# Performance work log

Measured on AMD Instinct MI355X. Metric: run time of the kernel, lower is better.

The kernel has to match this reference:

```python
import jax, jax.numpy as jnp
import numpy as np
from collections import deque

N, IN_DIM, H, B, L = 512, 64, 128, 256, 2
SOURCE = 105
E_UND = 2048


def _build_graph_and_masks():
    rng = np.random.default_rng(0)
    s = rng.integers(0, N, E_UND)
    d = rng.integers(0, N, E_UND)
    edge_index = np.stack([np.concatenate([s, d]), np.concatenate([d, s])]).astype(np.int32)
    # BFS depths from source (undirected)
    adj = [[] for _ in range(N)]
    for a, b in zip(edge_index[0], edge_index[1]):
        adj[int(a)].append(int(b))
    depths = np.full(N, np.inf)
    depths[SOURCE] = 0.0
    q = deque([SOURCE]); seen = {SOURCE}
    while q:
        u = q.popleft()
        for v in adj[u]:
            if v not in seen:
                seen.add(v); depths[v] = depths[u] + 1.0; q.append(v)
    finite = np.isfinite(depths)
    maxd = depths[finite].max() if finite.any() else 0.0
    depths[~finite] = maxd + 1.0
    adj_mask = np.zeros((N, N), np.float32)
    adj_mask[edge_index[0], edge_index[1]] = 1.0
    adj_mask[edge_index[1], edge_index[0]] = 1.0
    np.fill_diagonal(adj_mask, 1.0)
    direction_mask = (depths[None, :] <= depths[:, None]).astype(np.float32)
    # admittance_matrix is None -> uniform init, then masked
    initial_causal = (np.ones((N, N), np.float32) / N) * adj_mask * direction_mask
    return edge_index, adj_mask, direction_mask, initial_causal


def setup_inputs() -> dict:
    key = jax.random.key(0)
    ks = jax.random.split(key, 16)
    edge_index, adj_mask, direction_mask, initial_causal = _build_graph_and_masks()
    w = lambda k, shp: jax.random.normal(k, shp, jnp.float32) * 0.02
    return {
        'x': jax.random.normal(ks[0], (B, N, IN_DIM), jnp.float32),
        'edge_index': jnp.asarray(edge_index),
        'adj_mask': jnp.asarray(adj_mask),
        'direction_mask': jnp.asarray(direction_mask),
        'causal_logits': jnp.asarray(initial_causal),  # nn.Parameter init
        'W_in': w(ks[1], (IN_DIM, H)), 'b_in': jnp.zeros((H,), jnp.float32),
        'Wq': w(ks[2], (H, H)), 'bq': jnp.zeros((H,), jnp.float32),
        'Wk': w(ks[3], (H, H)), 'bk': jnp.zeros((H,), jnp.float32),
        'Wv': w(ks[4], (H, H)), 'bv': jnp.zeros((H,), jnp.float32),
        'gcn_W': w(ks[5], (L, H, H)), 'gcn_b': jnp.zeros((L, H), jnp.float32),
        'W_fuse': w(ks[6], (2 * H, H)), 'b_fuse': jnp.zeros((H,), jnp.float32),
        'ln_g': jnp.ones((H,), jnp.float32), 'ln_b': jnp.zeros((H,), jnp.float32),
    }


def reference(x, edge_index, adj_mask, direction_mask, causal_logits,
              W_in, b_in, Wq, bq, Wk, bk, Wv, bv,
              gcn_W, gcn_b, W_fuse, b_fuse, ln_g, ln_b):
    n = adj_mask.shape[0]
    h = jax.nn.relu(x @ W_in + b_in)                               # (B,N,H)

    # causal matrix: softmax over learned logits, physically masked, renormalized
    C = jax.nn.softmax(causal_logits, axis=-1) * adj_mask * direction_mask
    C = C / jnp.clip(C.sum(-1, keepdims=True), 1e-8)

    # masked causal attention
    Q = h @ Wq + bq; K = h @ Wk + bk; V = h @ Wv + bv
    scale = jnp.asarray(h.shape[-1] ** 0.5, h.dtype)
    attn = jax.nn.softmax(jnp.einsum('bnh,bmh->bnm', Q, K) / scale, axis=-1)
    attn = attn * C[None]
    attn = attn / (attn.sum(-1, keepdims=True) + 1e-8)
    h_causal = jnp.einsum('bnm,bmh->bnh', attn, V)

    # GCNConv stack (self-loops + symmetric norm; dropout is identity in eval)
    src = jnp.concatenate([edge_index[0], jnp.arange(n, dtype=edge_index.dtype)])
    dst = jnp.concatenate([edge_index[1], jnp.arange(n, dtype=edge_index.dtype)])
    deg = jnp.zeros((n,), h.dtype).at[dst].add(1.0)
    dinv = deg ** -0.5                                              # deg>=1 (self loops)
    norm = (dinv[src] * dinv[dst])[None, :, None]                   # (1,E+N,1)
    h_g = h
    for l in range(gcn_W.shape[0]):
        hW = h_g @ gcn_W[l]                                         # (B,N,H)
        msg = hW[:, src, :] * norm                                  # (B,E+N,H)
        h_g = jnp.zeros_like(hW).at[:, dst, :].add(msg) + gcn_b[l]
        h_g = jax.nn.relu(h_g)

    h_comb = jnp.concatenate([h_causal, h_g], axis=-1) @ W_fuse + b_fuse
    mu = h_comb.mean(-1, keepdims=True)
    var = ((h_comb - mu) ** 2).mean(-1, keepdims=True)
    out = (h_comb - mu) / jnp.sqrt(var + 1e-5) * ln_g + ln_b
    return out, C
```

## Files before the change

### kernel.cpp

```cpp
#include <hip/hip_runtime.h>
#include <hip/hip_bf16.h>
#include <math.h>

#define NN 512
#define HH 128
#define INDIM 64
#define BB 256
#define NE 4096
#define MROWS (BB*NN)
#define OUT0 (BB*NN*HH)

typedef __attribute__((ext_vector_type(8))) short short8v;
typedef __attribute__((ext_vector_type(4))) float float4v;

__device__ __forceinline__ unsigned short f2bf(float f) {
  unsigned u = __float_as_uint(f);
  unsigned r = (u + 0x7fffu + ((u >> 16) & 1u)) >> 16;
  return (unsigned short)r;
}
__device__ __forceinline__ float bf2f(unsigned short b) {
  return __uint_as_float(((unsigned)b) << 16);
}

__global__ __launch_bounds__(256) void k_causalC(
    const float* __restrict__ logits, const float* __restrict__ adj,
    const float* __restrict__ dir, float* __restrict__ Cout)
{
  const int row = blockIdx.x;
  const int t = threadIdx.x;
  __shared__ float red[256];
  const float* lrow = logits + (size_t)row * NN;
  float v0 = lrow[t], v1 = lrow[t + 256];
  float mx = fmaxf(v0, v1);
  red[t] = mx; __syncthreads();
  for (int s = 128; s > 0; s >>= 1) { if (t < s) red[t] = fmaxf(red[t], red[t + s]); __syncthreads(); }
  mx = red[0]; __syncthreads();
  float e0 = __expf(v0 - mx), e1 = __expf(v1 - mx);
  red[t] = e0 + e1; __syncthreads();
  for (int s = 128; s > 0; s >>= 1) { if (t < s) red[t] += red[t + s]; __syncthreads(); }
  float sumE = red[0]; __syncthreads();
  float m0 = adj[(size_t)row * NN + t] * dir[(size_t)row * NN + t];
  float m1 = adj[(size_t)row * NN + t + 256] * dir[(size_t)row * NN + t + 256];
  float me0 = e0 * m0, me1 = e1 * m1;
  red[t] = me0 + me1; __syncthreads();
  for (int s = 128; s > 0; s >>= 1) { if (t < s) red[t] += red[t + s]; __syncthreads(); }
  float sumME = red[0];
  float sm = sumME / sumE;
  float denom = fmaxf(sm, 1e-8f) * sumE;
  Cout[(size_t)row * NN + t]       = me0 / denom;
  Cout[(size_t)row * NN + t + 256] = me1 / denom;
}

__global__ __launch_bounds__(512) void k_csr(const int* __restrict__ ei,
                                             int* __restrict__ rp,
                                             int* __restrict__ ci,
                                             float* __restrict__ cw)
{
  __shared__ int scnt[512];
  __shared__ float sdinv[512];
  __shared__ int sval[512];
  __shared__ int scur[512];
  const int t = threadIdx.x;
  const int* src = ei;
  const int* dst = ei + NE;
  scnt[t] = 0;
  __syncthreads();
  for (int e = t; e < NE; e += 512) atomicAdd(&scnt[dst[e]], 1);
  __syncthreads();
  const int deg = scnt[t] + 1;
  sdinv[t] = rsqrtf((float)deg);
  sval[t] = deg;
  __syncthreads();
  for (int off = 1; off < 512; off <<= 1) {
    int add = (t >= off) ? sval[t - off] : 0;
    __syncthreads();
    sval[t] += add;
    __syncthreads();
  }
  const int excl = sval[t] - deg;
  rp[t] = excl;
  if (t == 511) rp[512] = excl + deg;
  ci[excl] = t;
  cw[excl] = sdinv[t] * sdinv[t];
  scur[t] = excl + 1;
  __syncthreads();
  for (int e = t; e < NE; e += 512) {
    int s = src[e], d = dst[e];
    int p = atomicAdd(&scur[d], 1);
    ci[p] = s;
    cw[p] = sdinv[s] * sdinv[d];
  }
}

__global__ __launch_bounds__(512) void k_ccsr(const int* __restrict__ ei,
                                              const float* __restrict__ Cmat,
                                              int* __restrict__ rp,
                                              int* __restrict__ ci,
                                              float* __restrict__ cw)
{
  __shared__ unsigned bm[512 * 16];
  __shared__ int cnt[512];
  __shared__ int sval[512];
  __shared__ int cur[512];
  const int t = threadIdx.x;
  const int* src = ei;
  const int* dst = ei + NE;
  for (int i = t; i < 512 * 16; i += 512) bm[i] = 0u;
  __syncthreads();
  bm[t * 16 + (t >> 5)] |= (1u << (t & 31));
  cnt[t] = 1;
  __syncthreads();
  for (int e = t; e < NE; e += 512) {
    int r = src[e], c = dst[e];
    if (Cmat[(size_t)r * NN + c] > 0.f) {
      unsigned bit = 1u << (c & 31);
      unsigned old = atomicOr(&bm[r * 16 + (c >> 5)], bit);
      if (!(old & bit)) atomicAdd(&cnt[r], 1);
    }
  }
  __syncthreads();
  const int myc = cnt[t];
  sval[t] = myc;
  __syncthreads();
  for (int off = 1; off < 512; off <<= 1) {
    int add = (t >= off) ? sval[t - off] : 0;
    __syncthreads();
    sval[t] += add;
    __syncthreads();
  }
  const int excl = sval[t] - myc;
  rp[t] = excl;
  if (t == 511) rp[512] = excl + myc;
  ci[excl] = t;
  cw[excl] = Cmat[(size_t)t * NN + t];
  cur[t] = excl + 1;
  bm[t * 16 + (t >> 5)] &= ~(1u << (t & 31));
  __syncthreads();
  for (int e = t; e < NE; e += 512) {
    int r = src[e], c = dst[e];
    if (Cmat[(size_t)r * NN + c] > 0.f) {
      unsigned bit = 1u << (c & 31);
      unsigned old = atomicAnd(&bm[r * 16 + (c >> 5)], ~bit);
      if (old & bit) {
        int p = atomicAdd(&cur[r], 1);
        ci[p] = c;
        cw[p] = Cmat[(size_t)r * NN + c];
      }
    }
  }
}

__device__ __forceinline__ void gcn_body(
    int bid, const unsigned short* __restrict__ hW,
    const int* __restrict__ rp, const int* __restrict__ ci,
    const float* __restrict__ cw, const float* __restrict__ bias,
    unsigned short* __restrict__ out, int OS, int OC0)
{
  const int i5 = bid >> 3;
  const int ng = i5 & 31;
  const int b = (bid & 7) * 32 + (i5 >> 5);
  const int t = threadIdx.x;
  const int node = ng * 16 + (t >> 4);
  const int f0 = (t & 15) * 8;

  float bcol[8];
  #pragma unroll
  for (int k = 0; k < 8; k++) bcol[k] = bias[f0 + k];

  const unsigned short* base = hW + (size_t)b * 512 * 128;
  const int beg = rp[node], end = rp[node + 1];
  float acc[8] = {0.f, 0.f, 0.f, 0.f, 0.f, 0.f, 0.f, 0.f};
  for (int j = beg; j < end; j++) {
    int s = ci[j];
    float w = cw[j];
    short8v v = *(const short8v*)&base[(size_t)s * 128 + f0];
    #pragma unroll
    for (int k = 0; k < 8; k++) acc[k] += w * bf2f((unsigned short)v[k]);
  }
  short8v o;
  #pragma unroll
  for (int k = 0; k < 8; k++) {
    float v = fmaxf(acc[k] + bcol[k], 0.f);
    o[k] = (short)f2bf(v);
  }
  *(short8v*)&out[((size_t)(b * 512 + node)) * OS + OC0 + f0] = o;
}

__global__ __launch_bounds__(256) void k_gcn(
    const unsigned short* __restrict__ hW,
    const int* __restrict__ rp, const int* __restrict__ ci,
    const float* __restrict__ cw, const float* __restrict__ bias,
    unsigned short* __restrict__ out, int OS, int OC0)
{
  gcn_body(blockIdx.x, hW, rp, ci, cw, bias, out, OS, OC0);
}

__device__ __forceinline__ void sattn_body(
    int bid, const unsigned short* __restrict__ Qbf,
    const unsigned short* __restrict__ Kbf, const unsigned short* __restrict__ Vbf,
    const int* __restrict__ rp, const int* __restrict__ ci,
    const float* __restrict__ cw, unsigned short* __restrict__ Ocb)
{
  const int i5 = bid >> 3;
  const int ng = i5 & 31;
  const int b = (bid & 7) * 32 + (i5 >> 5);
  const int t = threadIdx.x;
  const int node = ng * 16 + (t >> 4);
  const int f0 = (t & 15) * 8;
  const float scale = 0.088388347648318447f;

  const size_t rowq = ((size_t)(b * 512 + node)) * 128 + f0;
  short8v qv = *(const short8v*)&Qbf[rowq];
  float qf[8];
  #pragma unroll
  for (int k = 0; k < 8; k++) qf[k] = bf2f((unsigned short)qv[k]);

  const unsigned short* Kb = Kbf + (size_t)b * 512 * 128;
  const unsigned short* Vb = Vbf + (size_t)b * 512 * 128;
  const int beg = rp[node], end = rp[node + 1];
  float acc[8] = {0.f, 0.f, 0.f, 0.f, 0.f, 0.f, 0.f, 0.f};
  float sw = 0.f;
  int j = beg;
  float w0 = cw[j];
  int m = ci[j];
  short8v kv = *(const short8v*)&Kb[(size_t)m * 128 + f0];
  short8v vv = *(const short8v*)&Vb[(size_t)m * 128 + f0];
  for (; j < end; ) {
    const int jn = (j + 1 < end) ? j + 1 : j;
    const float w02 = cw[jn];
    const int m2 = ci[jn];
    short8v kv2 = *(const short8v*)&Kb[(size_t)m2 * 128 + f0];
    short8v vv2 = *(const short8v*)&Vb[(size_t)m2 * 128 + f0];
    float part = 0.f;
    #pragma unroll
    for (int k = 0; k < 8; k++) part += qf[k] * bf2f((unsigned short)kv[k]);
    part += __shfl_xor(part, 1);
    part += __shfl_xor(part, 2);
    part += __shfl_xor(part, 4);
    part += __shfl_xor(part, 8);
    float w = __expf(part * scale) * w0;
    sw += w;
    #pragma unroll
    for (int k = 0; k < 8; k++) acc[k] += w * bf2f((unsigned short)vv[k]);
    j++;
    w0 = w02; kv = kv2; vv = vv2;
  }
  float inv = 1.0f / sw;
  short8v o;
  #pragma unroll
  for (int k = 0; k < 8; k++) o[k] = (short)f2bf(acc[k] * inv);
  *(short8v*)&Ocb[((size_t)(b * 512 + node)) * 256 + f0] = o;
}

__global__ __launch_bounds__(256) void k_gs(
    const unsigned short* __restrict__ hW,
    const int* __restrict__ grp, const int* __restrict__ gci,
    const float* __restrict__ gcw, const float* __restrict__ gbias,
    const unsigned short* __restrict__ Qbf, const unsigned short* __restrict__ Kbf,
    const unsigned short* __restrict__ Vbf,
    const int* __restrict__ arp, const int* __restrict__ aci,
    const float* __restrict__ acw,
    unsigned short* __restrict__ Dout)
{
  if (blockIdx.x < 8192)
    gcn_body(blockIdx.x, hW, grp, gci, gcw, gbias, Dout, 256, 128);
  else
    sattn_body(blockIdx.x - 8192, Qbf, Kbf, Vbf, arp, aci, acw, Dout);
}

__global__ __launch_bounds__(256) void k_wt(
    const float* s0, const float* s1, const float* s2, const float* s3,
    const float* s4, const float* s5, const float* s6,
    unsigned short* d0, unsigned short* d1, unsigned short* d2, unsigned short* d3,
    unsigned short* d4, unsigned short* d5, unsigned short* d6)
{
  const float* srcs[7] = {s0, s1, s2, s3, s4, s5, s6};
  unsigned short* dsts[7] = {d0, d1, d2, d3, d4, d5, d6};
  const int Ks[7] = {64, 128, 128, 128, 128, 128, 256};
  const int j = blockIdx.x >> 3;
  const int nc = blockIdx.x & 7;
  const float* s = srcs[j];
  unsigned short* d = dsts[j];
  const int K = Ks[j];
  const int STRW = K + 8;
  const int n0 = nc * 16;
  __shared__ short tile[16 * 264];
  const int t = threadIdx.x;
  for (int i = t; i < K * 16; i += 256) {
    int k = i >> 4, nn = i & 15;
    tile[nn * STRW + k] = (short)f2bf(s[k * 128 + n0 + nn]);
  }
  __syncthreads();
  for (int i = t; i < K * 2; i += 256) {
    int nn = (i * 8) / K;
    int k  = (i * 8) % K;
    *(short8v*)&d[(size_t)(n0 + nn) * K + k] =
        *(const short8v*)&tile[nn * STRW + k];
  }
}

template<bool RELU>
__global__ __launch_bounds__(512) void k_wgemm(
    const unsigned short* __restrict__ Abf,
    const unsigned short* __restrict__ Wt,
    const float* __restrict__ bias,
    unsigned short* __restrict__ Out)
{
  constexpr int STR = 136;
  __shared__ short Ws[128 * STR];
  __shared__ short rep[8 * 2048];
  const int t = threadIdx.x;
  const int wave = t >> 6, lane = t & 63;
  const int l15 = lane & 15, quad = lane >> 4;
  short* rw = rep + wave * 2048;

  for (int i = t; i < 128 * 16; i += 512) {
    int n = i >> 4, seg = i & 15;
    *(short8v*)&Ws[n * STR + seg * 8] =
        *(const short8v*)&Wt[(size_t)n * 128 + seg * 8];
  }
  float bcol[8];
  #pragma unroll
  for (int nt = 0; nt < 8; nt++) bcol[nt] = bias ? bias[nt * 16 + l15] : 0.f;
  __syncthreads();

  const int nwaves = gridDim.x * 8;
  int tile = blockIdx.x * 8 + wave;
  short8v af[4], afn[4];
  if (tile < MROWS / 16) {
    #pragma unroll
    for (int dc = 0; dc < 4; dc++)
      af[dc] = *(const short8v*)&Abf[((size_t)(tile * 16 + l15)) * 128 + dc * 32 + quad * 8];
  }
  while (tile < MROWS / 16) {
    const int ntile = tile + nwaves;
    if (ntile < MROWS / 16) {
      #pragma unroll
      for (int dc = 0; dc < 4; dc++)
        afn[dc] = *(const short8v*)&Abf[((size_t)(ntile * 16 + l15)) * 128 + dc * 32 + quad * 8];
    }
    float4v acc[8];
    #pragma unroll
    for (int nt = 0; nt < 8; nt++) acc[nt] = (float4v){0.f, 0.f, 0.f, 0.f};
    #pragma unroll
    for (int k32 = 0; k32 < 4; k32++) {
      #pragma unroll
      for (int nt = 0; nt < 8; nt++) {
        short8v wf = *(const short8v*)&Ws[(nt * 16 + l15) * STR + k32 * 32 + quad * 8];
        acc[nt] = __builtin_amdgcn_mfma_f32_16x16x32_bf16(af[k32], wf, acc[nt], 0, 0, 0);
      }
    }
    #pragma unroll
    for (int nt = 0; nt < 8; nt++)
      #pragma unroll
      for (int r = 0; r < 4; r++) {
        float v = acc[nt][r] + bcol[nt];
        if (RELU) v = fmaxf(v, 0.f);
        rw[(quad * 4 + r) * 128 + nt * 16 + l15] = (short)f2bf(v);
      }
    asm volatile("s_waitcnt lgkmcnt(0)" ::: "memory");
    __builtin_amdgcn_sched_barrier(0);
    #pragma unroll
    for (int p = 0; p < 4; p++) {
      int row16 = (lane >> 4) + p * 4, seg = lane & 15;
      short8v vv = *(const short8v*)&rw[row16 * 128 + seg * 8];
      *(short8v*)&Out[((size_t)(tile * 16 + row16)) * 128 + seg * 8] = vv;
    }
    tile = ntile;
    #pragma unroll
    for (int dc = 0; dc < 4; dc++) af[dc] = afn[dc];
  }
}

#define GNT 4
template<int KD, bool RELU, bool BATCHW, int OMODE, bool AF32>
__global__ __launch_bounds__(256) void k_bgemm(
    const void* __restrict__ Ap, const unsigned short* __restrict__ Wt,
    const float* __restrict__ bias, void* __restrict__ Out, int OS,
    const float* __restrict__ lng, const float* __restrict__ lnb)
{
  constexpr int KCH = (KD < 128) ? KD : 128;
  constexpr int STR = KCH + 8;
  constexpr bool WONCE = (KD <= 128);
  constexpr int ASH = (64 * STR > 8192) ? 64 * STR : 8192;
  constexpr int TRIPS = KCH / 32;
  __shared__ short lds[ASH + 128 * STR];
  short* As = lds;
  short* Ws = lds + ASH;
  const unsigned short* Abf = (const unsigned short*)Ap;
  const float* Af = (const float*)Ap;
  const int t = threadIdx.x;
  const int wave = t >> 6, lane = t & 63;
  const int l15 = lane & 15, quad = lane >> 4;

  short8v ap[TRIPS];
  float4 fa[TRIPS], fb[TRIPS];

  auto LOADC = [&](int rb, int kc) {
    #pragma unroll
    for (int j = 0; j < TRIPS; j++) {
      int i = t + j * 256;
      int r = i / (KCH / 8), seg = i % (KCH / 8);
      if (AF32) {
        const float* sp = &Af[(size_t)(rb + r) * KD + kc + seg * 8];
        fa[j] = *(const float4*)sp;
        fb[j] = *(const float4*)(sp + 4);
      } else {
        int arow = BATCHW ? ((rb & 511) + r) : (rb + r);
        ap[j] = *(const short8v*)&Abf[(size_t)arow * KD + kc + seg * 8];
      }
    }
  };
  auto STOREC = [&]() {
    #pragma unroll
    for (int j = 0; j < TRIPS; j++) {
      int i = t + j * 256;
      int r = i / (KCH / 8), seg = i % (KCH / 8);
      if (AF32) {
        short8v pk;
        pk[0] = (short)f2bf(fa[j].x); pk[1] = (short)f2bf(fa[j].y);
        pk[2] = (short)f2bf(fa[j].z); pk[3] = (short)f2bf(fa[j].w);
        pk[4] = (short)f2bf(fb[j].x); pk[5] = (short)f2bf(fb[j].y);
        pk[6] = (short)f2bf(fb[j].z); pk[7] = (short)f2bf(fb[j].w);
        *(short8v*)&As[r * STR + seg * 8] = pk;
      } else {
        *(short8v*)&As[r * STR + seg * 8] = ap[j];
      }
    }
  };

  float bcol[8];
  #pragma unroll
  for (int nt = 0; nt < 8; nt++) bcol[nt] = bias ? bias[nt * 16 + l15] : 0.f;
  float gcol[8], bbcol[8];
  if (OMODE == 2) {
    #pragma unroll
    for (int nt = 0; nt < 8; nt++) { gcol[nt] = lng[nt * 16 + l15]; bbcol[nt] = lnb[nt * 16 + l15]; }
  }

  for (int g = blockIdx.x; g < (MROWS / 64) / GNT; g += gridDim.x) {
    if (WONCE) {
      const int b0 = (g * GNT * 64) >> 9;
      const unsigned short* Wb = BATCHW ? (Wt + (size_t)b0 * 128 * KD) : Wt;
      for (int i = t; i < 128 * (KCH / 8); i += 256) {
        int n = i / (KCH / 8), seg = i % (KCH / 8);
        *(short8v*)&Ws[n * STR + seg * 8] =
            *(const short8v*)&Wb[(size_t)n * KD + seg * 8];
      }
    }
    LOADC(g * GNT * 64, 0);
    for (int tt = 0; tt < GNT; tt++) {
      const int tile = g * GNT + tt;
      const int rowbase = tile * 64;
      const int b = rowbase >> 9;
      float4v acc[8];
      #pragma unroll
      for (int nt = 0; nt < 8; nt++) acc[nt] = (float4v){0.f, 0.f, 0.f, 0.f};

      for (int kc = 0; kc < KD; kc += KCH) {
        __syncthreads();
        STOREC();
        if (!WONCE) {
          const unsigned short* Wb = BATCHW ? (Wt + (size_t)b * 128 * KD) : Wt;
          for (int i = t; i < 128 * (KCH / 8); i += 256) {
            int n = i / (KCH / 8), seg = i % (KCH / 8);
            *(short8v*)&Ws[n * STR + seg * 8] =
                *(const short8v*)&Wb[(size_t)n * KD + kc + seg * 8];
          }
        }
        __syncthreads();
        {
          int nkc = kc + KCH, ntt = tt;
          if (nkc >= KD) { nkc = 0; ntt = tt + 1; }
          if (ntt < GNT) LOADC((g * GNT + ntt) * 64, nkc);
        }
        #pragma unroll
        for (int k32 = 0; k32 < KCH / 32; k32++) {
          short8v af = *(const short8v*)&As[(wave * 16 + l15) * STR + k32 * 32 + quad * 8];
          #pragma unroll
          for (int nt = 0; nt < 8; nt++) {
            short8v wf = *(const short8v*)&Ws[(nt * 16 + l15) * STR + k32 * 32 + quad * 8];
            acc[nt] = __builtin_amdgcn_mfma_f32_16x16x32_bf16(af, wf, acc[nt], 0, 0, 0);
          }
        }
      }

      __syncthreads();
      if (OMODE == 0) {
        short* rep = As + wave * 2048;
        #pragma unroll
        for (int nt = 0; nt < 8; nt++)
          #pragma unroll
          for (int r = 0; r < 4; r++) {
            float v = acc[nt][r] + bcol[nt];
            if (RELU) v = fmaxf(v, 0.f);
            rep[(quad * 4 + r) * 128 + nt * 16 + l15] = (short)f2bf(v);
          }
        __syncthreads();
        unsigned short* Ob = (unsigned short*)Out;
        #pragma unroll
        for (int p = 0; p < 4; p++) {
          int row16 = (lane >> 4) + p * 4, seg = lane & 15;
          short8v vv = *(const short8v*)&rep[row16 * 128 + seg * 8];
          *(short8v*)&Ob[(size_t)(rowbase + wave * 16 + row16) * OS + seg * 8] = vv;
        }
      } else if (OMODE == 1) {
        short* rep = As + wave * 2048;
        #pragma unroll
        for (int nt = 0; nt < 8; nt++)
          #pragma unroll
          for (int r = 0; r < 4; r++) {
            float v = acc[nt][r] + bcol[nt];
            if (RELU) v = fmaxf(v, 0.f);
            rep[(nt * 16 + l15) * 16 + quad * 4 + r] = (short)f2bf(v);
          }
        __syncthreads();
        unsigned short* Ob = (unsigned short*)Out;
        int node0 = (rowbase & 511) + wave * 16;
        #pragma unroll
        for (int p = 0; p < 4; p++) {
          int idx = p * 64 + lane, c = idx >> 1, half = idx & 1;
          short8v vv = *(const short8v*)&rep[c * 16 + half * 8];
          *(short8v*)&Ob[((size_t)(b * 128 + c)) * 512 + node0 + half * 8] = vv;
        }
      } else {
        float* repw = (float*)lds + wave * 2048;
        float vv[8][4];
        float s[4] = {0, 0, 0, 0}, ss[4] = {0, 0, 0, 0};
        #pragma unroll
        for (int nt = 0; nt < 8; nt++)
          #pragma unroll
          for (int r = 0; r < 4; r++) {
            float v = acc[nt][r] + bcol[nt];
            vv[nt][r] = v;
            s[r] += v; ss[r] += v * v;
          }
        #pragma unroll
        for (int r = 0; r < 4; r++) {
          s[r] += __shfl_xor(s[r], 1);  s[r] += __shfl_xor(s[r], 2);
          s[r] += __shfl_xor(s[r], 4);  s[r] += __shfl_xor(s[r], 8);
          ss[r] += __shfl_xor(ss[r], 1); ss[r] += __shfl_xor(ss[r], 2);
          ss[r] += __shfl_xor(ss[r], 4); ss[r] += __shfl_xor(ss[r], 8);
        }
        #pragma unroll
        for (int r = 0; r < 4; r++) {
          float mu = s[r] * (1.0f / 128.0f);
          float var = ss[r] * (1.0f / 128.0f) - mu * mu;
          float inv = rsqrtf(var + 1e-5f);
          #pragma unroll
          for (int nt = 0; nt < 8; nt++)
            repw[(quad * 4 + r) * 128 + nt * 16 + l15] =
                (vv[nt][r] - mu) * inv * gcol[nt] + bbcol[nt];
        }
        __syncthreads();
        float* Of = (float*)Out;
        #pragma unroll
        for (int p = 0; p < 8; p++) {
          int row16 = (lane >> 5) + p * 2, seg = lane & 31;
          float4 o = *(const float4*)&repw[row16 * 128 + seg * 4];
          *(float4*)&Of[(size_t)(rowbase + wave * 16 + row16) * 128 + seg * 4] = o;
        }
      }
    }
  }
}

__global__ __launch_bounds__(512) void k_hqkv4(
    const float* __restrict__ x,
    const unsigned short* __restrict__ Wint,
    const float* __restrict__ bin,
    const unsigned short* __restrict__ W0, const unsigned short* __restrict__ W1,
    const unsigned short* __restrict__ W2, const unsigned short* __restrict__ W3,
    const float* __restrict__ b1, const float* __restrict__ b2,
    const float* __restrict__ b3,
    unsigned short* __restrict__ O0, unsigned short* __restrict__ O1,
    unsigned short* __restrict__ O2, unsigned short* __restrict__ O3)
{
  constexpr int STR = 136;
  constexpr int RSTR = 136;
  __shared__ short Ws[128 * STR];
  __shared__ short rep[8 * 2304];
  const int t = threadIdx.x;
  const int wave = t >> 6, lane = t & 63;
  const int l15 = lane & 15, quad = lane >> 4;
  short* rw = rep + wave * 2304;

  const unsigned short* Wsrc[4] = {W0, W1, W2, W3};
  const float* Bsrc[4] = {nullptr, b1, b2, b3};
  unsigned short* Osrc[4] = {O0, O1, O2, O3};

  float bh[8];
  #pragma unroll
  for (int nt = 0; nt < 8; nt++) bh[nt] = bin[nt * 16 + l15];

  for (int g = blockIdx.x; g < MROWS / 256; g += gridDim.x) {
    __syncthreads();
    for (int i = t; i < 128 * 8; i += 512) {
      int n = i >> 3, seg = i & 7;
      *(short8v*)&Ws[n * STR + seg * 8] =
          *(const short8v*)&Wint[(size_t)n * 64 + seg * 8];
    }
    __syncthreads();

    short8v af_all[2][4];
    #pragma unroll
    for (int tt = 0; tt < 2; tt++) {
      const int row0 = (g * 2 + tt) * 128 + wave * 16;
      const float* xp = &x[(size_t)(row0 + l15) * 64 + quad * 16];
      float4 fx0 = *(const float4*)(xp);
      float4 fx1 = *(const float4*)(xp + 4);
      float4 fx2 = *(const float4*)(xp + 8);
      float4 fx3 = *(const float4*)(xp + 12);
      short8v px0, px1;
      px0[0] = (short)f2bf(fx0.x); px0[1] = (short)f2bf(fx0.y);
      px0[2] = (short)f2bf(fx0.z); px0[3] = (short)f2bf(fx0.w);
      px0[4] = (short)f2bf(fx1.x); px0[5] = (short)f2bf(fx1.y);
      px0[6] = (short)f2bf(fx1.z); px0[7] = (short)f2bf(fx1.w);
      px1[0] = (short)f2bf(fx2.x); px1[1] = (short)f2bf(fx2.y);
      px1[2] = (short)f2bf(fx2.z); px1[3] = (short)f2bf(fx2.w);
      px1[4] = (short)f2bf(fx3.x); px1[5] = (short)f2bf(fx3.y);
      px1[6] = (short)f2bf(fx3.z); px1[7] = (short)f2bf(fx3.w);
      *(short8v*)&rw[l15 * 72 + quad * 16]     = px0;
      *(short8v*)&rw[l15 * 72 + quad * 16 + 8] = px1;
      asm volatile("s_waitcnt lgkmcnt(0)" ::: "memory");
      __builtin_amdgcn_sched_barrier(0);

      float4v hacc[8];
      #pragma unroll
      for (int nt = 0; nt < 8; nt++) hacc[nt] = (float4v){0.f, 0.f, 0.f, 0.f};
      #pragma unroll
      for (int k32 = 0; k32 < 2; k32++) {
        short8v ax = *(const short8v*)&rw[l15 * 72 + k32 * 32 + quad * 8];
        #pragma unroll
        for (int nt = 0; nt < 8; nt++) {
          short8v wf = *(const short8v*)&Ws[(nt * 16 + l15) * STR + k32 * 32 + quad * 8];
          hacc[nt] = __builtin_amdgcn_mfma_f32_16x16x32_bf16(ax, wf, hacc[nt], 0, 0, 0);
        }
      }
      #pragma unroll
      for (int nt = 0; nt < 8; nt++)
        #pragma unroll
        for (int r = 0; r < 4; r++) {
          float v = fmaxf(hacc[nt][r] + bh[nt], 0.f);
          rw[(quad * 4 + r) * RSTR + nt * 16 + l15] = (short)f2bf(v);
        }
      asm volatile("s_waitcnt lgkmcnt(0)" ::: "memory");
      __builtin_amdgcn_sched_barrier(0);
      #pragma unroll
      for (int dc = 0; dc < 4; dc++)
        af_all[tt][dc] = *(const short8v*)&rw[l15 * RSTR + dc * 32 + quad * 8];
    }

    #pragma unroll
    for (int s = 0; s < 4; s++) {
      __syncthreads();
      for (int i = t; i < 128 * 16; i += 512) {
        int n = i >> 4, seg = i & 15;
        *(short8v*)&Ws[n * STR + seg * 8] =
            *(const short8v*)&Wsrc[s][(size_t)n * 128 + seg * 8];
      }
      float bcol[8];
      #pragma unroll
      for (int nt = 0; nt < 8; nt++) bcol[nt] = Bsrc[s] ? Bsrc[s][nt * 16 + l15] : 0.f;
      __syncthreads();

      #pragma unroll
      for (int tt = 0; tt < 2; tt++) {
        const int rowbase = (g * 2 + tt) * 128;
        float4v acc[8];
        #pragma unroll
        for (int nt = 0; nt < 8; nt++) acc[nt] = (float4v){0.f, 0.f, 0.f, 0.f};
        #pragma unroll
        for (int k32 = 0; k32 < 4; k32++) {
          #pragma unroll
          for (int nt = 0; nt < 8; nt++) {
            short8v wf = *(const short8v*)&Ws[(nt * 16 + l15) * STR + k32 * 32 + quad * 8];
            acc[nt] = __builtin_amdgcn_mfma_f32_16x16x32_bf16(af_all[tt][k32], wf, acc[nt], 0, 0, 0);
          }
        }
        #pragma unroll
        for (int nt = 0; nt < 8; nt++)
          #pragma unroll
          for (int r = 0; r < 4; r++) {
            float v = acc[nt][r] + bcol[nt];
            rw[(quad * 4 + r) * RSTR + nt * 16 + l15] = (short)f2bf(v);
          }
        asm volatile("s_waitcnt lgkmcnt(0)" ::: "memory");
        __builtin_amdgcn_sched_barrier(0);
        unsigned short* Ob = Osrc[s];
        #pragma unroll
        for (int p = 0; p < 4; p++) {
          int row16 = (lane >> 4) + p * 4, seg = lane & 15;
          short8v vv = *(const short8v*)&rw[row16 * RSTR + seg * 8];
          *(short8v*)&Ob[(size_t)(rowbase + wave * 16 + row16) * 128 + seg * 8] = vv;
        }
      }
    }
  }
}

extern "C" void kernel_launch(void* const* d_in, const int* in_sizes, int n_in,
                              void* d_out, int out_size, void* d_ws, size_t ws_size,
                              hipStream_t stream)
{
  const float* x     = (const float*)d_in[0];
  const int*   ei    = (const int*)d_in[1];
  const float* adj   = (const float*)d_in[2];
  const float* dmask = (const float*)d_in[3];
  const float* clog  = (const float*)d_in[4];
  const float* W_in  = (const float*)d_in[5];
  const float* b_in  = (const float*)d_in[6];
  const float* Wq    = (const float*)d_in[7];
  const float* bq    = (const float*)d_in[8];
  const float* Wk    = (const float*)d_in[9];
  const float* bk    = (const float*)d_in[10];
  const float* Wv    = (const float*)d_in[11];
  const float* bv    = (const float*)d_in[12];
  const float* gcnW  = (const float*)d_in[13];
  const float* gcnB  = (const float*)d_in[14];
  const float* Wf    = (const float*)d_in[15];
  const float* bf    = (const float*)d_in[16];
  const float* lng   = (const float*)d_in[17];
  const float* lnb   = (const float*)d_in[18];

  float* outp = (float*)d_out;
  float* Cmat = outp + OUT0;

  char* W = (char*)d_ws;
  const size_t SLOT = (size_t)MROWS * 128 * 2;
  unsigned short* A0 = (unsigned short*)(W);
  unsigned short* B0 = (unsigned short*)(W + SLOT);
  unsigned short* C0 = (unsigned short*)(W + 2 * SLOT);
  unsigned short* D0 = (unsigned short*)(W + 3 * SLOT);
  char* AUX = W + 5 * SLOT;
  int*   csr_rp = (int*)AUX;
  int*   csr_ci = csr_rp + 640;
  float* csr_cw = (float*)(csr_ci + 4608);
  int*   crp    = (int*)(AUX + 131072);
  int*   cci    = crp + 640;
  float* ccw    = (float*)(cci + 8192);
  unsigned short* WB    = (unsigned short*)(AUX + 512 * 512 * 4) + 512 * 512 * 2;
  unsigned short* W_int = WB;
  unsigned short* Wqt   = WB + 8192;
  unsigned short* Wkt   = Wqt + 16384;
  unsigned short* Wvt   = Wkt + 16384;
  unsigned short* G0t   = Wvt + 16384;
  unsigned short* G1t   = G0t + 16384;
  unsigned short* Wft   = G1t + 16384;

  unsigned short* Vbf = (unsigned short*)outp;
  unsigned short* E0  = Vbf + (size_t)MROWS * 128;

  k_causalC<<<512, 256, 0, stream>>>(clog, adj, dmask, Cmat);
  k_csr<<<1, 512, 0, stream>>>(ei, csr_rp, csr_ci, csr_cw);
  k_ccsr<<<1, 512, 0, stream>>>(ei, Cmat, crp, cci, ccw);
  k_wt<<<56, 256, 0, stream>>>(W_in, Wq, Wk, Wv, gcnW, gcnW + HH * HH, Wf,
                               W_int, Wqt, Wkt, Wvt, G0t, G1t, Wft);

  k_hqkv4<<<512, 512, 0, stream>>>(
      x, W_int, b_in, G0t, Wqt, Wkt, Wvt, bq, bk, bv, A0, C0, E0, Vbf);
  k_gcn<<<8192, 256, 0, stream>>>(A0, csr_rp, csr_ci, csr_cw, gcnB, B0, 128, 0);
  k_wgemm<false><<<512, 512, 0, stream>>>(B0, G1t, nullptr, A0);
  k_gs<<<16384, 256, 0, stream>>>(
      A0, csr_rp, csr_ci, csr_cw, gcnB + HH,
      C0, E0, Vbf, crp, cci, ccw, D0);
  k_bgemm<256, false, false, 2, false><<<512, 256, 0, stream>>>(
      D0, Wft, bf, outp, 128, lng, lnb);
}
```

Baseline: 364.5 us.

## Replace fusion GEMM+LayerNorm with wave-tiled kernel holding full weight in LDS

Replaces the templated block GEMM used for the fuse projection plus LayerNorm with a dedicated kernel. It loads the whole 128x256 weight into LDS once per block and has each wave own 16-row tiles, reading A fragments straight from global into registers. This removes per-tile syncthreads, A staging through LDS and the LDS repack before stores, at the cost of uncoalesced scalar fp32 output writes. The GCN gather loop is also software-pipelined to prefetch the next neighbor row.

Result: slower. 406.5 us (+11.5%).

```diff
diff --git a/kernel.cpp b/kernel.cpp
--- a/kernel.cpp
+++ b/kernel.cpp
@@ -170,18 +170,25 @@
   const unsigned short* base = hW + (size_t)b * 512 * 128;
   const int beg = rp[node], end = rp[node + 1];
   float acc[8] = {0.f, 0.f, 0.f, 0.f, 0.f, 0.f, 0.f, 0.f};
-  for (int j = beg; j < end; j++) {
-    int s = ci[j];
-    float w = cw[j];
-    short8v v = *(const short8v*)&base[(size_t)s * 128 + f0];
+  int j = beg;
+  float w = cw[j];
+  int m = ci[j];
+  short8v v = *(const short8v*)&base[(size_t)m * 128 + f0];
+  for (; j < end; ) {
+    const int jn = (j + 1 < end) ? j + 1 : j;
+    const float w2 = cw[jn];
+    const int m2 = ci[jn];
+    short8v v2 = *(const short8v*)&base[(size_t)m2 * 128 + f0];
     #pragma unroll
     for (int k = 0; k < 8; k++) acc[k] += w * bf2f((unsigned short)v[k]);
+    j++;
+    w = w2; v = v2;
   }
   short8v o;
   #pragma unroll
   for (int k = 0; k < 8; k++) {
-    float v = fmaxf(acc[k] + bcol[k], 0.f);
-    o[k] = (short)f2bf(v);
+    float vv = fmaxf(acc[k] + bcol[k], 0.f);
+    o[k] = (short)f2bf(vv);
   }
   *(short8v*)&out[((size_t)(b * 512 + node)) * OS + OC0 + f0] = o;
 }
@@ -372,195 +379,76 @@
   }
 }
 
-#define GNT 4
-template<int KD, bool RELU, bool BATCHW, int OMODE, bool AF32>
-__global__ __launch_bounds__(256) void k_bgemm(
-    const void* __restrict__ Ap, const unsigned short* __restrict__ Wt,
-    const float* __restrict__ bias, void* __restrict__ Out, int OS,
-    const float* __restrict__ lng, const float* __restrict__ lnb)
-{
-  constexpr int KCH = (KD < 128) ? KD : 128;
-  constexpr int STR = KCH + 8;
-  constexpr bool WONCE = (KD <= 128);
-  constexpr int ASH = (64 * STR > 8192) ? 64 * STR : 8192;
-  constexpr int TRIPS = KCH / 32;
-  __shared__ short lds[ASH + 128 * STR];
-  short* As = lds;
-  short* Ws = lds + ASH;
-  const unsigned short* Abf = (const unsigned short*)Ap;
-  const float* Af = (const float*)Ap;
+__global__ __launch_bounds__(512) void k_lngemm(
+    const unsigned short* __restrict__ Abf,
+    const unsigned short* __restrict__ Wt,
+    const float* __restrict__ bias,
+    const float* __restrict__ lng, const float* __restrict__ lnb,
+    float* __restrict__ Out)
+{
+  constexpr int STR = 264;
+  __shared__ short Ws[128 * STR];
   const int t = threadIdx.x;
   const int wave = t >> 6, lane = t & 63;
   const int l15 = lane & 15, quad = lane >> 4;
 
-  short8v ap[TRIPS];
-  float4 fa[TRIPS], fb[TRIPS];
-
-  auto LOADC = [&](int rb, int kc) {
-    #pragma unroll
-    for (int j = 0; j < TRIPS; j++) {
-      int i = t + j * 256;
-      int r = i / (KCH / 8), seg = i % (KCH / 8);
-      if (AF32) {
-        const float* sp = &Af[(size_t)(rb + r) * KD + kc + seg * 8];
-        fa[j] = *(const float4*)sp;
-        fb[j] = *(const float4*)(sp + 4);
-      } else {
-        int arow = BATCHW ? ((rb & 511) + r) : (rb + r);
-        ap[j] = *(const short8v*)&Abf[(size_t)arow * KD + kc + seg * 8];
-      }
-    }
-  };
-  auto STOREC = [&]() {
-    #pragma unroll
-    for (int j = 0; j < TRIPS; j++) {
-      int i = t + j * 256;
-      int r = i / (KCH / 8), seg = i % (KCH / 8);
-      if (AF32) {
-        short8v pk;
-        pk[0] = (short)f2bf(fa[j].x); pk[1] = (short)f2bf(fa[j].y);
-        pk[2] = (short)f2bf(fa[j].z); pk[3] = (short)f2bf(fa[j].w);
-        pk[4] = (short)f2bf(fb[j].x); pk[5] = (short)f2bf(fb[j].y);
-        pk[6] = (short)f2bf(fb[j].z); pk[7] = (short)f2bf(fb[j].w);
-        *(short8v*)&As[r * STR + seg * 8] = pk;
-      } else {
-        *(short8v*)&As[r * STR + seg * 8] = ap[j];
-      }
-    }
-  };
-
-  float bcol[8];
+  for (int i = t; i < 128 * 32; i += 512) {
+    int n = i >> 5, seg = i & 31;
+    *(short8v*)&Ws[n * STR + seg * 8] =
+        *(const short8v*)&Wt[(size_t)n * 256 + seg * 8];
+  }
+  float bcol[8], gcol[8], bbcol[8];
   #pragma unroll
-  for (int nt = 0; nt < 8; nt++) bcol[nt] = bias ? bias[nt * 16 + l15] : 0.f;
-  float gcol[8], bbcol[8];
-  if (OMODE == 2) {
-    #pragma unroll
-    for (int nt = 0; nt < 8; nt++) { gcol[nt] = lng[nt * 16 + l15]; bbcol[nt] = lnb[nt * 16 + l15]; }
-  }
-
-  for (int g = blockIdx.x; g < (MROWS / 64) / GNT; g += gridDim.x) {
-    if (WONCE) {
-      const int b0 = (g * GNT * 64) >> 9;
-      const unsigned short* Wb = BATCHW ? (Wt + (size_t)b0 * 128 * KD) : Wt;
-      for (int i = t; i < 128 * (KCH / 8); i += 256) {
-        int n = i / (KCH / 8), seg = i % (KCH / 8);
-        *(short8v*)&Ws[n * STR + seg * 8] =
-            *(const short8v*)&Wb[(size_t)n * KD + seg * 8];
-      }
-    }
-    LOADC(g * GNT * 64, 0);
-    for (int tt = 0; tt < GNT; tt++) {
-      const int tile = g * GNT + tt;
-      const int rowbase = tile * 64;
-      const int b = rowbase >> 9;
-      float4v acc[8];
-      #pragma unroll
-      for (int nt = 0; nt < 8; nt++) acc[nt] = (float4v){0.f, 0.f, 0.f, 0.f};
-
-      for (int kc = 0; kc < KD; kc += KCH) {
-        __syncthreads();
-        STOREC();
-        if (!WONCE) {
-          const unsigned short* Wb = BATCHW ? (Wt + (size_t)b * 128 * KD) : Wt;
-          for (int i = t; i < 128 * (KCH / 8); i += 256) {
-            int n = i / (KCH / 8), seg = i % (KCH / 8);
-            *(short8v*)&Ws[n * STR + seg * 8] =
-                *(const short8v*)&Wb[(size_t)n * KD + kc + seg * 8];
-          }
-        }
-        __syncthreads();
-        {
-          int nkc = kc + KCH, ntt = tt;
-          if (nkc >= KD) { nkc = 0; ntt = tt + 1; }
-          if (ntt < GNT) LOADC((g * GNT + ntt) * 64, nkc);
-        }
-        #pragma unroll
-        for (int k32 = 0; k32 < KCH / 32; k32++) {
-          short8v af = *(const short8v*)&As[(wave * 16 + l15) * STR + k32 * 32 + quad * 8];
-          #pragma unroll
-          for (int nt = 0; nt < 8; nt++) {
-            short8v wf = *(const short8v*)&Ws[(nt * 16 + l15) * STR + k32 * 32 + quad * 8];
-            acc[nt] = __builtin_amdgcn_mfma_f32_16x16x32_bf16(af, wf, acc[nt], 0, 0, 0);
-          }
-        }
-      }
-
-      __syncthreads();
-      if (OMODE == 0) {
-        short* rep = As + wave * 2048;
-        #pragma unroll
-        for (int nt = 0; nt < 8; nt++)
-          #pragma unroll
-          for (int r = 0; r < 4; r++) {
-            float v = acc[nt][r] + bcol[nt];
-            if (RELU) v = fmaxf(v, 0.f);
-            rep[(quad * 4 + r) * 128 + nt * 16 + l15] = (short)f2bf(v);
-          }
-        __syncthreads();
-        unsigned short* Ob = (unsigned short*)Out;
-        #pragma unroll
-        for (int p = 0; p < 4; p++) {
-          int row16 = (lane >> 4) + p * 4, seg = lane & 15;
-          short8v vv = *(const short8v*)&rep[row16 * 128 + seg * 8];
-          *(short8v*)&Ob[(size_t)(rowbase + wave * 16 + row16) * OS + seg * 8] = vv;
-        }
-      } else if (OMODE == 1) {
-        short* rep = As + wave * 2048;
-        #pragma unroll
-        for (int nt = 0; nt < 8; nt++)
-          #pragma unroll
-          for (int r = 0; r < 4; r++) {
-            float v = acc[nt][r] + bcol[nt];
-            if (RELU) v = fmaxf(v, 0.f);
-            rep[(nt * 16 + l15) * 16 + quad * 4 + r] = (short)f2bf(v);
-          }
-        __syncthreads();
-        unsigned short* Ob = (unsigned short*)Out;
-        int node0 = (rowbase & 511) + wave * 16;
-        #pragma unroll
-        for (int p = 0; p < 4; p++) {
-          int idx = p * 64 + lane, c = idx >> 1, half = idx & 1;
-          short8v vv = *(const short8v*)&rep[c * 16 + half * 8];
-          *(short8v*)&Ob[((size_t)(b * 128 + c)) * 512 + node0 + half * 8] = vv;
-        }
-      } else {
-        float* repw = (float*)lds + wave * 2048;
-        float vv[8][4];
-        float s[4] = {0, 0, 0, 0}, ss[4] = {0, 0, 0, 0};
-        #pragma unroll
-        for (int nt = 0; nt < 8; nt++)
-          #pragma unroll
-          for (int r = 0; r < 4; r++) {
-            float v = acc[nt][r] + bcol[nt];
-            vv[nt][r] = v;
-            s[r] += v; ss[r] += v * v;
-          }
-        #pragma unroll
-        for (int r = 0; r < 4; r++) {
-          s[r] += __shfl_xor(s[r], 1);  s[r] += __shfl_xor(s[r], 2);
-          s[r] += __shfl_xor(s[r], 4);  s[r] += __shfl_xor(s[r], 8);
-          ss[r] += __shfl_xor(ss[r], 1); ss[r] += __shfl_xor(ss[r], 2);
-          ss[r] += __shfl_xor(ss[r], 4); ss[r] += __shfl_xor(ss[r], 8);
-        }
-        #pragma unroll
-        for (int r = 0; r < 4; r++) {
-          float mu = s[r] * (1.0f / 128.0f);
-          float var = ss[r] * (1.0f / 128.0f) - mu * mu;
-          float inv = rsqrtf(var + 1e-5f);
-          #pragma unroll
-          for (int nt = 0; nt < 8; nt++)
-            repw[(quad * 4 + r) * 128 + nt * 16 + l15] =
-                (vv[nt][r] - mu) * inv * gcol[nt] + bbcol[nt];
-        }
-        __syncthreads();
-        float* Of = (float*)Out;
-        #pragma unroll
-        for (int p = 0; p < 8; p++) {
-          int row16 = (lane >> 5) + p * 2, seg = lane & 31;
-          float4 o = *(const float4*)&repw[row16 * 128 + seg * 4];
-          *(float4*)&Of[(size_t)(rowbase + wave * 16 + row16) * 128 + seg * 4] = o;
-        }
-      }
+  for (int nt = 0; nt < 8; nt++) {
+    bcol[nt]  = bias[nt * 16 + l15];
+    gcol[nt]  = lng[nt * 16 + l15];
+    bbcol[nt] = lnb[nt * 16 + l15];
+  }
+  __syncthreads();
+
+  const int nwaves = gridDim.x * 8;
+  for (int tile = blockIdx.x * 8 + wave; tile < MROWS / 16; tile += nwaves) {
+    short8v af[8];
+    #pragma unroll
+    for (int dc = 0; dc < 8; dc++)
+      af[dc] = *(const short8v*)&Abf[((size_t)(tile * 16 + l15)) * 256 + dc * 32 + quad * 8];
+    float4v acc[8];
+    #pragma unroll
+    for (int nt = 0; nt < 8; nt++) acc[nt] = (float4v){0.f, 0.f, 0.f, 0.f};
+    #pragma unroll
+    for (int k32 = 0; k32 < 8; k32++) {
+      #pragma unroll
+      for (int nt = 0; nt < 8; nt++) {
+        short8v wf = *(const short8v*)&Ws[(nt * 16 + l15) * STR + k32 * 32 + quad * 8];
+        acc[nt] = __builtin_amdgcn_mfma_f32_16x16x32_bf16(af[k32], wf, acc[nt], 0, 0, 0);
+      }
+    }
+    float vv[8][4];
+    float s[4] = {0, 0, 0, 0}, ss[4] = {0, 0, 0, 0};
+    #pragma unroll
+    for (int nt = 0; nt < 8; nt++)
+      #pragma unroll
+      for (int r = 0; r < 4; r++) {
+        float v = acc[nt][r] + bcol[nt];
+        vv[nt][r] = v;
+        s[r] += v; ss[r] += v * v;
+      }
+    #pragma unroll
+    for (int r = 0; r < 4; r++) {
+      s[r] += __shfl_xor(s[r], 1);  s[r] += __shfl_xor(s[r], 2);
+      s[r] += __shfl_xor(s[r], 4);  s[r] += __shfl_xor(s[r], 8);
+      ss[r] += __shfl_xor(ss[r], 1); ss[r] += __shfl_xor(ss[r], 2);
+      ss[r] += __shfl_xor(ss[r], 4); ss[r] += __shfl_xor(ss[r], 8);
+    }
+    #pragma unroll
+    for (int r = 0; r < 4; r++) {
+      float mu = s[r] * (1.0f / 128.0f);
+      float var = ss[r] * (1.0f / 128.0f) - mu * mu;
+      float inv = rsqrtf(var + 1e-5f);
+      const size_t rowoff = ((size_t)(tile * 16 + quad * 4 + r)) * 128;
+      #pragma unroll
+      for (int nt = 0; nt < 8; nt++)
+        Out[rowoff + nt * 16 + l15] = (vv[nt][r] - mu) * inv * gcol[nt] + bbcol[nt];
     }
   }
 }
@@ -764,6 +652,5 @@
   k_gs<<<16384, 256, 0, stream>>>(
       A0, csr_rp, csr_ci, csr_cw, gcnB + HH,
       C0, E0, Vbf, crp, cci, ccw, D0);
-  k_bgemm<256, false, false, 2, false><<<512, 256, 0, stream>>>(
-      D0, Wft, bf, outp, 128, lng, lnb);
-}
+  k_lngemm<<<512, 512, 0, stream>>>(D0, Wft, bf, lng, lnb, outp);
+}
```
